# Performance work log

Measured on AMD Instinct MI355X. Metric: run time of the kernel, lower is better.

Reference implementation:

```python
import jax, jax.numpy as jnp
import numpy as np

FILTER_SZ = 5  # matches init_kwargs filter_sz


def setup_inputs() -> dict:
    key = jax.random.key(0)
    image = jax.random.normal(key, (16, 3, 512, 512), dtype=jnp.float32)
    return {"image": image}


def reference(image):
    # scipy.ndimage.median_filter with default mode='reflect' ((d c b a | a b c d)),
    # which corresponds to jnp.pad mode='symmetric'.
    k = FILTER_SZ
    pad = k // 2
    B, C, H, W = image.shape
    padded = jnp.pad(image, ((0, 0), (0, 0), (pad, pad), (pad, pad)), mode="symmetric")
    # Gather all k*k shifted views: [B, C, H, W, k*k]. Fixed small loop over the
    # window offsets (k*k = 25), fully vectorized over batch/channel/spatial dims.
    patches = jnp.stack(
        [padded[:, :, i:i + H, j:j + W] for i in range(k) for j in range(k)],
        axis=-1,
    )
    # Order statistic: median of the k*k window per pixel.
    return jnp.median(patches, axis=-1)
```

## Files before the change

kernel.cpp:

```cpp
#include <hip/hip_runtime.h>


typedef _Float16 h2 __attribute__((ext_vector_type(2)));

static __device__ __forceinline__ h2 h2min(h2 a, h2 b) { return __builtin_elementwise_min(a, b); }
static __device__ __forceinline__ h2 h2max(h2 a, h2 b) { return __builtin_elementwise_max(a, b); }

static __device__ __forceinline__ h2 pack2(float a, float b) {
    return __builtin_bit_cast(h2, __builtin_amdgcn_cvt_pkrtz(a, b));
}

#define CAS(a, b) do { h2 _mn = h2min((a), (b)); (b) = h2max((a), (b)); (a) = _mn; } while (0)

static __device__ __forceinline__ void sort5(h2 &e0, h2 &e1, h2 &e2, h2 &e3, h2 &e4) {
    CAS(e0, e1); CAS(e3, e4); CAS(e2, e4); CAS(e2, e3); CAS(e0, e3);
    CAS(e0, e2); CAS(e1, e4); CAS(e1, e3); CAS(e1, e2);
}

#define MINMAX8(w0, w1, w2, w3, w4, w5, w6, w7) do {      \
    CAS(w0, w1); CAS(w2, w3); CAS(w4, w5); CAS(w6, w7);   \
    CAS(w0, w2); CAS(w4, w6); CAS(w0, w4);                \
    CAS(w1, w3); CAS(w5, w7); CAS(w3, w7); } while (0)

#define MINMAX5(v0, v1, v2, v3, v4) do {                  \
    CAS(v0, v1); CAS(v2, v3); CAS(v0, v2); CAS(v1, v3);   \
    CAS(v0, v4); CAS(v3, v4); } while (0)

static __device__ __forceinline__ h2 med3h(h2 a, h2 b, h2 c) {
    return h2max(h2min(a, b), h2min(h2max(a, b), c));
}

static __device__ __forceinline__ h2 sel7of13(h2 c0, h2 c1, h2 c2, h2 c3, h2 c4, h2 c5, h2 c6,
                                              h2 c7, h2 c8, h2 c9, h2 c10, h2 c11, h2 c12) {
    MINMAX8(c0, c1, c2, c3, c4, c5, c6, c7); c0 = c8;  c7 = c9;
    MINMAX8(c0, c1, c2, c3, c4, c5, c6, c7); c0 = c10; c7 = c11;
    MINMAX8(c0, c1, c2, c3, c4, c5, c6, c7); c0 = c12;
    MINMAX5(c0, c1, c2, c3, c4); c0 = c5; c4 = c6;
    MINMAX5(c0, c1, c2, c3, c4);
    return med3h(c1, c2, c3);
}

static __device__ __forceinline__ int refl(int v, int n) {
    v = (v < 0) ? (-v - 1) : v;
    return (v >= n) ? (2 * n - 1 - v) : v;
}

constexpr int W = 512, H = 512, R = 8, PX = 4;

__global__ __launch_bounds__(256) void median5x5_kernel(const float* __restrict__ in,
                                                        float* __restrict__ out) {
    const int tx = blockIdx.x * 64 + threadIdx.x;
    const int x0 = PX * tx;
    const int ystrip = blockIdx.y * 4 + threadIdx.y;
    const int y0 = ystrip * R;
    const size_t plane = (size_t)blockIdx.z * ((size_t)H * W);
    const float* __restrict__ p = in + plane;
    float* __restrict__ q = out + plane;

    const bool swapA = (x0 == 0);
    const bool swapD = (x0 == W - PX);
    const int aB = swapA ? 0 : x0 - 2;
    const int dB = swapD ? x0 + 2 : x0 + 4;

    auto load_raw = [&](int y, float (&f)[8]) {
        const float* __restrict__ rp = p + (size_t)refl(y, H) * W;
        float2 a = *reinterpret_cast<const float2*>(rp + aB);
        float2 b = *reinterpret_cast<const float2*>(rp + x0);
        float2 c = *reinterpret_cast<const float2*>(rp + (x0 + 2));
        float2 d = *reinterpret_cast<const float2*>(rp + dB);
        f[0] = swapA ? a.y : a.x;
        f[1] = swapA ? a.x : a.y;
        f[2] = b.x; f[3] = b.y; f[4] = c.x; f[5] = c.y;
        f[6] = swapD ? d.y : d.x;
        f[7] = swapD ? d.x : d.y;
    };

    auto pack_sort2 = [&](h2 (&dA)[5], h2 (&dB_)[5], const float (&f)[8]) {
        h2 w1 = pack2(f[1], f[2]);
        h2 w2 = pack2(f[2], f[3]);
        h2 w3 = pack2(f[3], f[4]);
        h2 w4 = pack2(f[4], f[5]);
        dA[0] = pack2(f[0], f[1]); dA[1] = w1; dA[2] = w2; dA[3] = w3; dA[4] = w4;
        dB_[0] = w2; dB_[1] = w3; dB_[2] = w4;
        dB_[3] = pack2(f[5], f[6]); dB_[4] = pack2(f[6], f[7]);
        sort5(dA[0], dA[1], dA[2], dA[3], dA[4]);
        sort5(dB_[0], dB_[1], dB_[2], dB_[3], dB_[4]);
    };

    auto median_of = [&](h2 (&s0)[5], h2 (&s1)[5], h2 (&s2)[5],
                         h2 (&s3)[5], h2 (&s4)[5]) -> h2 {
        h2 a0=s0[0], a1=s1[0], a2=s2[0], a3=s3[0], a4=s4[0]; sort5(a0,a1,a2,a3,a4);
        h2 b0=s0[1], b1=s1[1], b2=s2[1], b3=s3[1], b4=s4[1]; sort5(b0,b1,b2,b3,b4);
        h2 c0=s0[2], c1=s1[2], c2=s2[2], c3=s3[2], c4=s4[2]; sort5(c0,c1,c2,c3,c4);
        h2 d0=s0[3], d1=s1[3], d2=s2[3], d3=s3[3], d4=s4[3]; sort5(d0,d1,d2,d3,d4);
        h2 e0=s0[4], e1=s1[4], e2=s2[4], e3=s3[4], e4=s4[4]; sort5(e0,e1,e2,e3,e4);
        (void)a0; (void)a1; (void)a2; (void)b0; (void)b1; (void)c0; (void)c4;
        (void)d3; (void)d4; (void)e2; (void)e3; (void)e4;
        return sel7of13(d0, e0, c1, d1, e1, b2, c2, d2, a3, b3, c3, a4, b4);
    };

    h2 rowsA[5][5], rowsB[5][5];

    #pragma unroll
    for (int k = 0; k < 4; ++k) {
        float f[8];
        load_raw(y0 - 2 + k, f);
        pack_sort2(rowsA[k], rowsB[k], f);
    }

    float cf[8];
    load_raw(y0 + 2, cf);

    #pragma unroll
    for (int t = 0; t < R; ++t) {
        pack_sort2(rowsA[(4 + t) % 5], rowsB[(4 + t) % 5], cf);
        if (t < R - 1) load_raw(y0 + 3 + t, cf);

        h2 medA = median_of(rowsA[(t + 0) % 5], rowsA[(t + 1) % 5], rowsA[(t + 2) % 5],
                            rowsA[(t + 3) % 5], rowsA[(t + 4) % 5]);
        h2 medB = median_of(rowsB[(t + 0) % 5], rowsB[(t + 1) % 5], rowsB[(t + 2) % 5],
                            rowsB[(t + 3) % 5], rowsB[(t + 4) % 5]);

        float4 o;
        o.x = (float)medA.x;
        o.y = (float)medA.y;
        o.z = (float)medB.x;
        o.w = (float)medB.y;
        *reinterpret_cast<float4*>(q + (size_t)(y0 + t) * W + x0) = o;
    }
}

extern "C" void kernel_launch(void* const* d_in, const int* in_sizes, int n_in,
                              void* d_out, int out_size, void* d_ws, size_t ws_size,
                              hipStream_t stream) {
    const float* in = (const float*)d_in[0];
    float* out = (float*)d_out;
    dim3 block(64, 4, 1);
    dim3 grid(512 / (64 * PX), 512 / (4 * R), 16 * 3);
    hipLaunchKernelGGL(median5x5_kernel, grid, block, 0, stream, in, out);
}
```

Baseline: 118.8 us.

## Share column sorts across vertically adjacent outputs and prune selection network

Each loop iteration now produces two output rows. The four shared window rows are sorted per column once, and the outgoing or incoming row's element is then inserted by partial insertion, which computes only the ranks the selection needs. The 7-of-13 selection is rewritten to start with a few pre-comparisons that shrink the later min/max passes. The aim is to cut the ALU compare count per output, in exchange for more live registers from the six-row ring and two row buffers.

```diff
diff --git a/kernel.cpp b/kernel.cpp
--- a/kernel.cpp
+++ b/kernel.cpp
@@ -30,14 +30,21 @@
     return h2max(h2min(a, b), h2min(h2max(a, b), c));
 }
 
-static __device__ __forceinline__ h2 sel7of13(h2 c0, h2 c1, h2 c2, h2 c3, h2 c4, h2 c5, h2 c6,
-                                              h2 c7, h2 c8, h2 c9, h2 c10, h2 c11, h2 c12) {
-    MINMAX8(c0, c1, c2, c3, c4, c5, c6, c7); c0 = c8;  c7 = c9;
-    MINMAX8(c0, c1, c2, c3, c4, c5, c6, c7); c0 = c10; c7 = c11;
-    MINMAX8(c0, c1, c2, c3, c4, c5, c6, c7); c0 = c12;
-    MINMAX5(c0, c1, c2, c3, c4); c0 = c5; c4 = c6;
-    MINMAX5(c0, c1, c2, c3, c4);
-    return med3h(c1, c2, c3);
+static __device__ __forceinline__ h2 sel7of13_ds(h2 d0, h2 e0, h2 c1, h2 d1, h2 e1,
+                                                 h2 b2, h2 c2, h2 d2,
+                                                 h2 a3, h2 b3, h2 c3, h2 a4, h2 b4) {
+    CAS(c1, b2);
+    CAS(d0, c1);
+    CAS(e1, d2);
+    h2 w0 = a3, w1 = d1, w2 = e0, w3 = e1, w4 = c1, w5 = c2, w6 = b2, w7 = b3;
+    MINMAX8(w0, w1, w2, w3, w4, w5, w6, w7);
+    w0 = c3; w7 = a4;
+    MINMAX8(w0, w1, w2, w3, w4, w5, w6, w7);
+    w0 = b4;
+    MINMAX5(w0, w1, w2, w3, w4);
+    w0 = w5; w4 = w6;
+    MINMAX5(w0, w1, w2, w3, w4);
+    return med3h(w1, w2, w3);
 }
 
 static __device__ __forceinline__ int refl(int v, int n) {
@@ -87,19 +94,70 @@
         sort5(dB_[0], dB_[1], dB_[2], dB_[3], dB_[4]);
     };
 
-    auto median_of = [&](h2 (&s0)[5], h2 (&s1)[5], h2 (&s2)[5],
-                         h2 (&s3)[5], h2 (&s4)[5]) -> h2 {
-        h2 a0=s0[0], a1=s1[0], a2=s2[0], a3=s3[0], a4=s4[0]; sort5(a0,a1,a2,a3,a4);
-        h2 b0=s0[1], b1=s1[1], b2=s2[1], b3=s3[1], b4=s4[1]; sort5(b0,b1,b2,b3,b4);
-        h2 c0=s0[2], c1=s1[2], c2=s2[2], c3=s3[2], c4=s4[2]; sort5(c0,c1,c2,c3,c4);
-        h2 d0=s0[3], d1=s1[3], d2=s2[3], d3=s3[3], d4=s4[3]; sort5(d0,d1,d2,d3,d4);
-        h2 e0=s0[4], e1=s1[4], e2=s2[4], e3=s3[4], e4=s4[4]; sort5(e0,e1,e2,e3,e4);
-        (void)a0; (void)a1; (void)a2; (void)b0; (void)b1; (void)c0; (void)c4;
-        (void)d3; (void)d4; (void)e2; (void)e3; (void)e4;
-        return sel7of13(d0, e0, c1, d1, e1, b2, c2, d2, a3, b3, c3, a4, b4);
-    };
-
-    h2 rowsA[5][5], rowsB[5][5];
+    auto ins_top2 = [&](h2 g2, h2 g3, h2 x, h2 &p3, h2 &p4) {
+        h2 u3 = h2min(g3, x); p4 = h2max(g3, x); p3 = h2max(g2, u3);
+    };
+    auto ins_top3 = [&](h2 g1, h2 g2, h2 g3, h2 x, h2 &p2, h2 &p3, h2 &p4) {
+        h2 u3 = h2min(g3, x); p4 = h2max(g3, x); p3 = h2max(g2, u3);
+        h2 u2 = h2min(g2, u3); p2 = h2max(g1, u2);
+    };
+    auto ins_mid3 = [&](h2 g0, h2 g1, h2 g2, h2 g3, h2 x, h2 &p1, h2 &p2, h2 &p3) {
+        h2 u3 = h2min(g3, x); p3 = h2max(g2, u3);
+        h2 u2 = h2min(g2, u3); p2 = h2max(g1, u2);
+        h2 u1 = h2min(g1, u2); p1 = h2max(g0, u1);
+    };
+    auto ins_bot3 = [&](h2 g0, h2 g1, h2 g2, h2 x, h2 &p0, h2 &p1, h2 &p2) {
+        p0 = h2min(g0, x); h2 t1 = h2max(g0, x);
+        p1 = h2min(g1, t1); h2 t2 = h2max(g1, t1);
+        p2 = h2min(g2, t2);
+    };
+    auto ins_bot2 = [&](h2 g0, h2 g1, h2 x, h2 &p0, h2 &p1) {
+        p0 = h2min(g0, x); p1 = h2min(g1, h2max(g0, x));
+    };
+
+    auto pair_medians = [&](h2 (&s0)[5], h2 (&s1)[5], h2 (&s2)[5], h2 (&s3)[5],
+                            h2 (&s4)[5], h2 (&s5)[5], h2 &mT, h2 &mU) {
+        h2 Td0,Te0,Tc1,Td1,Te1,Tb2,Tc2,Td2,Ta3,Tb3,Tc3,Ta4,Tb4;
+        h2 Ud0,Ue0,Uc1,Ud1,Ue1,Ub2,Uc2,Ud2,Ua3,Ub3,Uc3,Ua4,Ub4;
+        {
+            h2 g0=s1[0], g1=s2[0], g2=s3[0], g3=s4[0];
+            CAS(g0,g1); CAS(g2,g3); CAS(g0,g2); CAS(g1,g3); CAS(g1,g2);
+            ins_top2(g2, g3, s0[0], Ta3, Ta4);
+            ins_top2(g2, g3, s5[0], Ua3, Ua4);
+            (void)g0;
+        }
+        {
+            h2 g0=s1[1], g1=s2[1], g2=s3[1], g3=s4[1];
+            CAS(g0,g1); CAS(g2,g3); CAS(g0,g2); CAS(g1,g3); CAS(g1,g2);
+            ins_top3(g1, g2, g3, s0[1], Tb2, Tb3, Tb4);
+            ins_top3(g1, g2, g3, s5[1], Ub2, Ub3, Ub4);
+            (void)g0;
+        }
+        {
+            h2 g0=s1[2], g1=s2[2], g2=s3[2], g3=s4[2];
+            CAS(g0,g1); CAS(g2,g3); CAS(g0,g2); CAS(g1,g3); CAS(g1,g2);
+            ins_mid3(g0, g1, g2, g3, s0[2], Tc1, Tc2, Tc3);
+            ins_mid3(g0, g1, g2, g3, s5[2], Uc1, Uc2, Uc3);
+        }
+        {
+            h2 g0=s1[3], g1=s2[3], g2=s3[3], g3=s4[3];
+            CAS(g0,g1); CAS(g2,g3); CAS(g0,g2); CAS(g1,g3); CAS(g1,g2);
+            ins_bot3(g0, g1, g2, s0[3], Td0, Td1, Td2);
+            ins_bot3(g0, g1, g2, s5[3], Ud0, Ud1, Ud2);
+            (void)g3;
+        }
+        {
+            h2 g0=s1[4], g1=s2[4], g2=s3[4], g3=s4[4];
+            CAS(g0,g1); CAS(g2,g3); CAS(g0,g2); CAS(g1,g3); CAS(g1,g2);
+            ins_bot2(g0, g1, s0[4], Te0, Te1);
+            ins_bot2(g0, g1, s5[4], Ue0, Ue1);
+            (void)g2; (void)g3;
+        }
+        mT = sel7of13_ds(Td0,Te0,Tc1,Td1,Te1,Tb2,Tc2,Td2,Ta3,Tb3,Tc3,Ta4,Tb4);
+        mU = sel7of13_ds(Ud0,Ue0,Uc1,Ud1,Ue1,Ub2,Uc2,Ud2,Ua3,Ub3,Uc3,Ua4,Ub4);
+    };
+
+    h2 rowsA[6][5], rowsB[6][5];
 
     #pragma unroll
     for (int k = 0; k < 4; ++k) {
@@ -108,25 +166,33 @@
         pack_sort2(rowsA[k], rowsB[k], f);
     }
 
-    float cf[8];
-    load_raw(y0 + 2, cf);
+    float cfA[8], cfB[8];
+    load_raw(y0 + 2, cfA);
+    load_raw(y0 + 3, cfB);
 
     #pragma unroll
-    for (int t = 0; t < R; ++t) {
-        pack_sort2(rowsA[(4 + t) % 5], rowsB[(4 + t) % 5], cf);
-        if (t < R - 1) load_raw(y0 + 3 + t, cf);
-
-        h2 medA = median_of(rowsA[(t + 0) % 5], rowsA[(t + 1) % 5], rowsA[(t + 2) % 5],
-                            rowsA[(t + 3) % 5], rowsA[(t + 4) % 5]);
-        h2 medB = median_of(rowsB[(t + 0) % 5], rowsB[(t + 1) % 5], rowsB[(t + 2) % 5],
-                            rowsB[(t + 3) % 5], rowsB[(t + 4) % 5]);
-
-        float4 o;
-        o.x = (float)medA.x;
-        o.y = (float)medA.y;
-        o.z = (float)medB.x;
-        o.w = (float)medB.y;
-        *reinterpret_cast<float4*>(q + (size_t)(y0 + t) * W + x0) = o;
+    for (int i = 0; i < 4; ++i) {
+        const int cur = y0 + 2 * i;
+        pack_sort2(rowsA[(2*i + 4) % 6], rowsB[(2*i + 4) % 6], cfA);
+        if (i < 3) load_raw(cur + 4, cfA);
+        pack_sort2(rowsA[(2*i + 5) % 6], rowsB[(2*i + 5) % 6], cfB);
+        if (i < 3) load_raw(cur + 5, cfB);
+
+        h2 mA0, mA1, mB0, mB1;
+        pair_medians(rowsA[(2*i + 0) % 6], rowsA[(2*i + 1) % 6], rowsA[(2*i + 2) % 6],
+                     rowsA[(2*i + 3) % 6], rowsA[(2*i + 4) % 6], rowsA[(2*i + 5) % 6],
+                     mA0, mA1);
+        pair_medians(rowsB[(2*i + 0) % 6], rowsB[(2*i + 1) % 6], rowsB[(2*i + 2) % 6],
+                     rowsB[(2*i + 3) % 6], rowsB[(2*i + 4) % 6], rowsB[(2*i + 5) % 6],
+                     mB0, mB1);
+
+        float4 o0, o1;
+        o0.x = (float)mA0.x; o0.y = (float)mA0.y;
+        o0.z = (float)mB0.x; o0.w = (float)mB0.y;
+        o1.x = (float)mA1.x; o1.y = (float)mA1.y;
+        o1.z = (float)mB1.x; o1.w = (float)mB1.y;
+        *reinterpret_cast<float4*>(q + (size_t)cur * W + x0) = o0;
+        *reinterpret_cast<float4*>(q + (size_t)(cur + 1) * W + x0) = o1;
     }
 }
 
```

Result: faster. 112.5 us (-5.3%).
